# Kernel optimization log

Hardware: AMD Instinct MI355X
Metric: run time of the kernel (lower is better)

The kernel has to match this reference:

```python
import jax, jax.numpy as jnp
import numpy as np

NUM_SPLITS = 4
SPLIT_CH = 4          # 16 channels / 4 splits
N_BRANCH = NUM_SPLITS * 2   # 2 pyramid branches per group
K = 2                 # multi_frequency_compression k
MAX_U, MAX_V = 5, 5
N_CLASSES = 60
LN_EPS = 1e-5


def _conv(x, w):
    # x: [B, Cin, H, W], w: [Cout, Cin, kh, kw], SAME padding, stride 1
    return jax.lax.conv_general_dilated(
        x, w, window_strides=(1, 1), padding='SAME',
        dimension_numbers=('NCHW', 'OIHW', 'NCHW'))


def _branch(x, w3, b3, w5, b5, w7, b7):
    # one PyramidMultiScaleCNN branch: dense 3x3 -> 5x5 -> 7x7 with input re-concat
    a = jax.nn.relu(_conv(x, w3) + b3[None, :, None, None])            # [B,64,H,W]
    b = jax.nn.relu(_conv(jnp.concatenate([a, x], 1), w5) + b5[None, :, None, None])  # [B,128,H,W]
    c = jax.nn.relu(_conv(jnp.concatenate([b, x], 1), w7) + b7[None, :, None, None])  # [B,256,H,W]
    return jnp.concatenate([a, b, c], axis=1)                          # [B,448,H,W]


def _dct_basis(H, W, dtype):
    # first K frequency pairs (u,v) in row-major order of a MAX_U x MAX_V grid
    uv = [(i // MAX_V, i % MAX_V) for i in range(K)]
    u = jnp.array([p[0] for p in uv], dtype=dtype)   # [K]
    v = jnp.array([p[1] for p in uv], dtype=dtype)   # [K]
    h = jnp.arange(H, dtype=dtype) + 0.5
    w = jnp.arange(W, dtype=dtype) + 0.5
    cos_u = jnp.cos(jnp.pi * u[:, None] * h[None, :] / H)  # [K,H]
    cos_v = jnp.cos(jnp.pi * v[:, None] * w[None, :] / W)  # [K,W]
    return cos_u, cos_v


def setup_inputs() -> dict:
    key = jax.random.key(0)
    ks = jax.random.split(key, 16)
    B, C, H, W = 16, 16, 32, 32
    s = 0.02
    x = jax.random.normal(ks[0], (B, C, H, W), jnp.float32)
    # stacked params for the 8 identical-shaped pyramid branches (index = 2*group + branch)
    w3 = jax.random.normal(ks[1], (N_BRANCH, 64, SPLIT_CH, 3, 3), jnp.float32) * s
    b3 = jnp.zeros((N_BRANCH, 64), jnp.float32)
    w5 = jax.random.normal(ks[2], (N_BRANCH, 128, 64 + SPLIT_CH, 5, 5), jnp.float32) * s
    b5 = jnp.zeros((N_BRANCH, 128), jnp.float32)
    w7 = jax.random.normal(ks[3], (N_BRANCH, 256, 128 + SPLIT_CH, 7, 7), jnp.float32) * s
    b7 = jnp.zeros((N_BRANCH, 256), jnp.float32)
    fused_c = N_BRANCH * 448  # 3584
    Wg = jax.random.normal(ks[4], (N_CLASSES, fused_c), jnp.float32) * s
    bg = jnp.zeros((N_CLASSES,), jnp.float32)
    f_dct = fused_c * K       # 7168
    gamma = jnp.ones((f_dct,), jnp.float32)
    beta = jnp.zeros((f_dct,), jnp.float32)
    Wd = jax.random.normal(ks[5], (N_CLASSES, f_dct), jnp.float32) * s
    bd = jnp.zeros((N_CLASSES,), jnp.float32)
    return {"x": x, "w3": w3, "b3": b3, "w5": w5, "b5": b5, "w7": w7, "b7": b7,
            "Wg": Wg, "bg": bg, "gamma": gamma, "beta": beta, "Wd": Wd, "bd": bd}


def reference(x, w3, b3, w5, b5, w7, b7, Wg, bg, gamma, beta, Wd, bd):
    B, C, H, W = x.shape
    # split channels into groups: [NUM_SPLITS, B, SPLIT_CH, H, W]
    parts = x.reshape(B, NUM_SPLITS, SPLIT_CH, H, W).transpose(1, 0, 2, 3, 4)
    # each group feeds 2 branches; branch index i = 2*group + branch matches fused cat order
    xg = jnp.repeat(parts, 2, axis=0)                               # [8,B,SPLIT_CH,H,W]
    outs = jax.vmap(_branch)(xg, w3, b3, w5, b5, w7, b7)            # [8,B,448,H,W]
    fused = outs.transpose(1, 0, 2, 3, 4).reshape(B, N_BRANCH * 448, H, W)  # [B,3584,H,W]

    # GAP head
    gap_feat = fused.mean(axis=(2, 3))                              # [B,3584]
    gap_pred = gap_feat @ Wg.T + bg                                 # [B,60]

    # batched multi-frequency DCT compression (replaces per-sample Python loop)
    cos_u, cos_v = _dct_basis(H, W, fused.dtype)                    # [K,H],[K,W]
    dct = jnp.einsum('bchw,kh,kw->bck', fused, cos_u, cos_v)        # [B,3584,K]
    dct = dct.reshape(B, -1)                                        # [B,7168]

    mu = dct.mean(axis=-1, keepdims=True)
    var = jnp.var(dct, axis=-1, keepdims=True)
    normed = (dct - mu) * jax.lax.rsqrt(var + LN_EPS) * gamma + beta
    # dropout omitted (eval mode)
    dct_pred = normed @ Wd.T + bd                                   # [B,60]
    return (gap_pred, dct_pred)
```

## Files before the change

kernel.cpp:

```cpp
#include <hip/hip_runtime.h>
#include <math.h>

#define PI_F 3.14159265358979323846f

typedef short bf16x8 __attribute__((ext_vector_type(8)));
typedef float f32x4  __attribute__((ext_vector_type(4)));
typedef float f32x16 __attribute__((ext_vector_type(16)));

__device__ __forceinline__ short f2bf(float f) {
    union { float f; unsigned u; } v; v.f = f;
    unsigned r = v.u + 0x7fffu + ((v.u >> 16) & 1u);
    return (short)(r >> 16);
}


__global__ __launch_bounds__(256) void prep_s1in(const float* __restrict__ x, short* __restrict__ dst) {
    int idx = blockIdx.x * 256 + threadIdx.x;
    if (idx >= 64 * 1024) return;
    int px = idx & 1023;
    int g  = (idx >> 10) & 3;
    int b  = idx >> 12;
    short v8[8];
    #pragma unroll
    for (int j = 0; j < 8; ++j) {
        float f = (j < 4) ? x[((b * 16 + g * 4 + j) << 10) + px] : 0.f;
        v8[j] = f2bf(f);
    }
    *(int4*)(dst + (size_t)idx * 8) = *(const int4*)v8;
}

__global__ __launch_bounds__(256) void prep_sx(const float* __restrict__ x, short* __restrict__ dst,
                                               int CHS, int CH0) {
    int idx = blockIdx.x * 256 + threadIdx.x;
    if (idx >= 128 * 1024) return;
    int px = idx & 1023, pair = idx >> 10;
    int i = pair >> 4, b = pair & 15, g = i >> 1;
    short v8[8];
    #pragma unroll
    for (int j = 0; j < 8; ++j) {
        float f = (j < 4) ? x[((b * 16 + g * 4 + j) << 10) + px] : 0.f;
        v8[j] = f2bf(f);
    }
    *(int4*)(dst + (size_t)idx * CHS + CH0) = *(const int4*)v8;
}

template<int KS, int CHS, int CINR, int COUT, int NCH>
__global__ __launch_bounds__(256) void wprep_d(const float* __restrict__ w, short* __restrict__ Bw) {
    constexpr int TOTAL = 8 * KS * NCH * COUT * 4;
    int idx = blockIdx.x * 256 + threadIdx.x;
    if (idx >= TOTAL) return;
    int kb = idx & 3;
    int r  = idx >> 2;
    int n  = r % COUT;  r /= COUT;
    int c  = r % NCH;   r /= NCH;
    int kh = r % KS;
    int br = r / KS;
    short v8[8];
    #pragma unroll
    for (int j = 0; j < 8; ++j) {
        int k   = c * 32 + kb * 8 + j;
        int kwc = k / CHS;
        int ch  = k - kwc * CHS;
        float f = (kwc < KS && ch < CINR)
                ? w[(((size_t)br * COUT + n) * CINR + ch) * (KS * KS) + kh * KS + kwc] : 0.f;
        v8[j] = f2bf(f);
    }
    *(int4*)(Bw + (size_t)idx * 8) = *(const int4*)v8;
}

template<int KS, int CHS, int COUT, int CHS_OUT, int FOFF, bool S1SRC>
__global__ __launch_bounds__(512, 2) void conv_hk(
    const short* __restrict__ sIn,
    short* __restrict__ sOut,
    const short* __restrict__ Bw,
    const float* __restrict__ bias,
    float* __restrict__ sums)
{
    constexpr int PAD    = KS / 2;
    constexpr int NCH    = (KS * CHS + 31) / 32;
    constexpr int TCX    = 32 + (NCH * 32 - 1) / CHS;
    constexpr int NSLOT  = 9;
    constexpr int NFN    = COUT / 64;
    constexpr int CPP    = CHS / 8;
    constexpr int RCHK   = TCX * CPP;
    constexpr int CHUNKB = COUT * 32;
    static_assert(NCH == 1 || (NCH % 2) == 0, "NCH must be 1 or even");

    __shared__ int4 AtileV[(NSLOT * TCX * CHS) / 8];
    short* Atile = (short*)AtileV;

    const int t    = threadIdx.x;
    const int lane = t & 63, w = t >> 6;
    const int wm = w >> 2, wn = w & 3;
    const int lm = lane & 15, kb = lane >> 4;

    const int bid = blockIdx.x;
    const int i  = bid & 7;
    const int b  = (bid >> 3) & 15;
    const int mt = bid >> 7;
    const int r0 = mt * 8;

    const int pairPx = (i * 16 + b) << 10;
    const int srcPx  = S1SRC ? ((b * 4 + (i >> 1)) << 10) : pairPx;

    int nIdx[NFN], nOff[NFN];
    #pragma unroll
    for (int fn = 0; fn < NFN; ++fn) {
        nIdx[fn] = wn * (COUT / 4) + fn * 16 + lm;
        nOff[fn] = nIdx[fn] * 32 + kb * 8;
    }

    f32x4 acc[8][NFN];
    #pragma unroll
    for (int fm = 0; fm < 8; ++fm)
        #pragma unroll
        for (int fn = 0; fn < NFN; ++fn)
            acc[fm][fn] = (f32x4){0.f, 0.f, 0.f, 0.f};

    const short* Bp = Bw + (size_t)i * KS * NCH * CHUNKB;
    bf16x8 b0[NFN], b1[NFN];
    #pragma unroll
    for (int fn = 0; fn < NFN; ++fn)
        b0[fn] = *(const bf16x8*)(Bp + nOff[fn]);

    for (int e = t; e < 9 * RCHK; e += 512) {
        int j  = e / RCHK, e2 = e - j * RCHK;
        int tc = e2 / CPP, kc = e2 - tc * CPP;
        int rin = r0 - PAD + j, cin = tc - PAD;
        int4 v = {0, 0, 0, 0};
        if (rin >= 0 && rin < 32 && cin >= 0 && cin < 32)
            v = *(const int4*)(sIn + (size_t)(srcPx + rin * 32 + cin) * CHS + kc * 8);
        *(int4*)(Atile + (j * TCX + tc) * CHS + kc * 8) = v;
    }
    __syncthreads();

    for (int kh = 0; kh < KS; ++kh) {
        int aB[8];
        #pragma unroll
        for (int fm = 0; fm < 8; ++fm) {
            int slot = kh + wm * 4 + (fm >> 1);
            if (slot >= NSLOT) slot -= NSLOT;
            aB[fm] = (slot * TCX + (fm & 1) * 16 + lm) * CHS + kb * 8;
        }

        const bool doStage = (kh <= KS - 3);
        const int stRin = r0 - PAD + kh + 9;
        int4 stg0 = {0, 0, 0, 0};
        if (doStage) {
            if (t < RCHK) {
                int tc = t / CPP, kc = t - tc * CPP;
                int cin = tc - PAD;
                if (stRin >= 0 && stRin < 32 && cin >= 0 && cin < 32)
                    stg0 = *(const int4*)(sIn + (size_t)(srcPx + stRin * 32 + cin) * CHS + kc * 8);
            }
        }

        if constexpr (NCH == 1) {
            __builtin_amdgcn_s_setprio(1);
            #pragma unroll
            for (int fm = 0; fm < 8; ++fm) {
                bf16x8 af = *(const bf16x8*)(Atile + aB[fm]);
                #pragma unroll
                for (int fn = 0; fn < NFN; ++fn)
                    acc[fm][fn] = __builtin_amdgcn_mfma_f32_16x16x32_bf16(af, b0[fn], acc[fm][fn], 0, 0, 0);
            }
            __builtin_amdgcn_s_setprio(0);
            if (kh < KS - 1) {
                #pragma unroll
                for (int fn = 0; fn < NFN; ++fn)
                    b0[fn] = *(const bf16x8*)(Bp + CHUNKB + nOff[fn]);
            }
            Bp += CHUNKB;
        } else {
            #pragma unroll 1
            for (int c = 0; c < NCH; c += 2) {
                #pragma unroll
                for (int fn = 0; fn < NFN; ++fn)
                    b1[fn] = *(const bf16x8*)(Bp + (size_t)(c + 1) * CHUNKB + nOff[fn]);
                __builtin_amdgcn_s_setprio(1);
                #pragma unroll
                for (int fm = 0; fm < 8; ++fm) {
                    bf16x8 af = *(const bf16x8*)(Atile + aB[fm] + c * 32);
                    #pragma unroll
                    for (int fn = 0; fn < NFN; ++fn)
                        acc[fm][fn] = __builtin_amdgcn_mfma_f32_16x16x32_bf16(af, b0[fn], acc[fm][fn], 0, 0, 0);
                }
                __builtin_amdgcn_s_setprio(0);
                if (!(kh == KS - 1 && c + 2 >= NCH)) {
                    #pragma unroll
                    for (int fn = 0; fn < NFN; ++fn)
                        b0[fn] = *(const bf16x8*)(Bp + (size_t)(c + 2) * CHUNKB + nOff[fn]);
                }
                __builtin_amdgcn_s_setprio(1);
                #pragma unroll
                for (int fm = 0; fm < 8; ++fm) {
                    bf16x8 af = *(const bf16x8*)(Atile + aB[fm] + (c + 1) * 32);
                    #pragma unroll
                    for (int fn = 0; fn < NFN; ++fn)
                        acc[fm][fn] = __builtin_amdgcn_mfma_f32_16x16x32_bf16(af, b1[fn], acc[fm][fn], 0, 0, 0);
                }
                __builtin_amdgcn_s_setprio(0);
            }
            Bp += (size_t)NCH * CHUNKB;
        }

        __syncthreads();
        if (doStage) {
            if (t < RCHK) {
                int tc = t / CPP, kc = t - tc * CPP;
                *(int4*)(Atile + (kh * TCX + tc) * CHS + kc * 8) = stg0;
            }
        }
    }

    float cwv[2][4];
    #pragma unroll
    for (int half = 0; half < 2; ++half)
        #pragma unroll
        for (int r = 0; r < 4; ++r)
            cwv[half][r] = cosf(PI_F * (half * 16 + kb * 4 + r + 0.5f) / 32.f);

    #pragma unroll
    for (int fn = 0; fn < NFN; ++fn) {
        int n = nIdx[fn];
        float bv = bias[i * COUT + n];
        float s0 = 0.f, s1 = 0.f;
        #pragma unroll
        for (int fm = 0; fm < 8; ++fm) {
            int imgrow = wm * 4 + (fm >> 1);
            int half = fm & 1;
            #pragma unroll
            for (int r = 0; r < 4; ++r) {
                float v = fmaxf(acc[fm][fn][r] + bv, 0.f);
                if constexpr (CHS_OUT > 0) {
                    int col = half * 16 + kb * 4 + r;
                    int R = r0 + imgrow;
                    sOut[(size_t)(pairPx + R * 32 + col) * CHS_OUT + n] = f2bf(v);
                }
                s0 += v;
                s1 += v * cwv[half][r];
            }
        }
        s0 += __shfl_xor(s0, 16); s1 += __shfl_xor(s1, 16);
        s0 += __shfl_xor(s0, 32); s1 += __shfl_xor(s1, 32);
        if (kb == 0) {
            int ch = i * 448 + FOFF + n;
            atomicAdd(&sums[((size_t)b * 3584 + ch) * 2 + 0], s0);
            atomicAdd(&sums[((size_t)b * 3584 + ch) * 2 + 1], s1);
        }
    }
}

template<int KS, int CHS, int COUT, int CHS_OUT, int FOFF>
__global__ __launch_bounds__(512, 2) void conv_hk32(
    const short* __restrict__ sIn,
    short* __restrict__ sOut,
    const short* __restrict__ Bw,
    const float* __restrict__ bias,
    float* __restrict__ sums)
{
    constexpr int PAD    = KS / 2;
    constexpr int NCH    = (KS * CHS + 31) / 32;
    constexpr int TCX    = 32 + (NCH * 32 - 1) / CHS;
    constexpr int NSLOT  = 9;
    constexpr int NFN    = COUT / 128;
    constexpr int CPP    = CHS / 8;
    constexpr int RCHK   = TCX * CPP;
    constexpr int CHUNKB = COUT * 32;
    static_assert((NCH % 2) == 0, "NCH must be even");

    __shared__ int4 AtileV[(NSLOT * TCX * CHS) / 8];
    char* Alds = (char*)AtileV;

    const int t    = threadIdx.x;
    const int lane = t & 63, w = t >> 6;
    const int wm = w >> 2, wn = w & 3;
    const int ln = lane & 31, hi = lane >> 5;

    const int bid = blockIdx.x;
    const int i  = bid & 7;
    const int b  = (bid >> 3) & 15;
    const int mt = bid >> 7;
    const int r0 = mt * 8;
    const int pairPx = (i * 16 + b) << 10;

    int nIdx[NFN], nOff[NFN];
    #pragma unroll
    for (int fn = 0; fn < NFN; ++fn) {
        nIdx[fn] = wn * (COUT / 4) + fn * 32 + ln;
        nOff[fn] = nIdx[fn] * 32 + hi * 8;
    }

    f32x16 acc[4][NFN];
    #pragma unroll
    for (int mf = 0; mf < 4; ++mf)
        #pragma unroll
        for (int fn = 0; fn < NFN; ++fn)
            acc[mf][fn] = (f32x16)(0.f);

    const short* Bp = Bw + (size_t)i * KS * NCH * CHUNKB;
    bf16x8 b0[NFN][2], b1[NFN][2];
    #pragma unroll
    for (int fn = 0; fn < NFN; ++fn) {
        b0[fn][0] = *(const bf16x8*)(Bp + nOff[fn]);
        b0[fn][1] = *(const bf16x8*)(Bp + nOff[fn] + 16);
    }

    for (int e = t; e < 9 * RCHK; e += 512) {
        int j  = e / RCHK, e2 = e - j * RCHK;
        int tc = e2 / CPP, kc = e2 - tc * CPP;
        int rin = r0 - PAD + j, cin = tc - PAD;
        int4 v = {0, 0, 0, 0};
        if (rin >= 0 && rin < 32 && cin >= 0 && cin < 32)
            v = *(const int4*)(sIn + (size_t)(pairPx + rin * 32 + cin) * CHS + kc * 8);
        int off = ((j * TCX + tc) * CHS + kc * 8) * 2;
        off ^= ((off >> 7) & 1) << 4;
        *(int4*)(Alds + off) = v;
    }
    __syncthreads();

    for (int kh = 0; kh < KS; ++kh) {
        int aB[4];
        #pragma unroll
        for (int mf = 0; mf < 4; ++mf) {
            int slot = kh + wm * 4 + mf;
            if (slot >= NSLOT) slot -= NSLOT;
            aB[mf] = (slot * TCX + ln) * CHS * 2 + hi * 16;
        }

        const bool doStage = (kh <= KS - 3);
        const int stRin = r0 - PAD + kh + 9;
        int4 stg0 = {0, 0, 0, 0}, stg1 = {0, 0, 0, 0};
        if (doStage) {
            if (t < RCHK) {
                int tc = t / CPP, kc = t - tc * CPP;
                int cin = tc - PAD;
                if (stRin >= 0 && stRin < 32 && cin >= 0 && cin < 32)
                    stg0 = *(const int4*)(sIn + (size_t)(pairPx + stRin * 32 + cin) * CHS + kc * 8);
            }
            if constexpr (RCHK > 512) {
                int e2 = t + 512;
                if (e2 < RCHK) {
                    int tc = e2 / CPP, kc = e2 - tc * CPP;
                    int cin = tc - PAD;
                    if (stRin >= 0 && stRin < 32 && cin >= 0 && cin < 32)
                        stg1 = *(const int4*)(sIn + (size_t)(pairPx + stRin * 32 + cin) * CHS + kc * 8);
                }
            }
        }

        #pragma unroll 1
        for (int c = 0; c < NCH; c += 2) {
            #pragma unroll
            for (int fn = 0; fn < NFN; ++fn) {
                b1[fn][0] = *(const bf16x8*)(Bp + (size_t)(c + 1) * CHUNKB + nOff[fn]);
                b1[fn][1] = *(const bf16x8*)(Bp + (size_t)(c + 1) * CHUNKB + nOff[fn] + 16);
            }
            __builtin_amdgcn_s_setprio(1);
            #pragma unroll
            for (int kk = 0; kk < 2; ++kk) {
                #pragma unroll
                for (int mf = 0; mf < 4; ++mf) {
                    int off = aB[mf] + c * 64 + kk * 32;
                    off ^= ((off >> 7) & 1) << 4;
                    bf16x8 af = *(const bf16x8*)(Alds + off);
                    #pragma unroll
                    for (int fn = 0; fn < NFN; ++fn)
                        acc[mf][fn] = __builtin_amdgcn_mfma_f32_32x32x16_bf16(af, b0[fn][kk], acc[mf][fn], 0, 0, 0);
                }
            }
            __builtin_amdgcn_s_setprio(0);
            if (!(kh == KS - 1 && c + 2 >= NCH)) {
                #pragma unroll
                for (int fn = 0; fn < NFN; ++fn) {
                    b0[fn][0] = *(const bf16x8*)(Bp + (size_t)(c + 2) * CHUNKB + nOff[fn]);
                    b0[fn][1] = *(const bf16x8*)(Bp + (size_t)(c + 2) * CHUNKB + nOff[fn] + 16);
                }
            }
            __builtin_amdgcn_s_setprio(1);
            #pragma unroll
            for (int kk = 0; kk < 2; ++kk) {
                #pragma unroll
                for (int mf = 0; mf < 4; ++mf) {
                    int off = aB[mf] + (c + 1) * 64 + kk * 32;
                    off ^= ((off >> 7) & 1) << 4;
                    bf16x8 af = *(const bf16x8*)(Alds + off);
                    #pragma unroll
                    for (int fn = 0; fn < NFN; ++fn)
                        acc[mf][fn] = __builtin_amdgcn_mfma_f32_32x32x16_bf16(af, b1[fn][kk], acc[mf][fn], 0, 0, 0);
                }
            }
            __builtin_amdgcn_s_setprio(0);
        }
        Bp += (size_t)NCH * CHUNKB;

        __syncthreads();
        if (doStage) {
            if (t < RCHK) {
                int tc = t / CPP, kc = t - tc * CPP;
                int off = ((kh * TCX + tc) * CHS + kc * 8) * 2;
                off ^= ((off >> 7) & 1) << 4;
                *(int4*)(Alds + off) = stg0;
            }
            if constexpr (RCHK > 512) {
                int e2 = t + 512;
                if (e2 < RCHK) {
                    int tc = e2 / CPP, kc = e2 - tc * CPP;
                    int off = ((kh * TCX + tc) * CHS + kc * 8) * 2;
                    off ^= ((off >> 7) & 1) << 4;
                    *(int4*)(Alds + off) = stg1;
                }
            }
        }
    }

    float cw[16];
    #pragma unroll
    for (int r = 0; r < 16; ++r) {
        int px = (r & 3) + 8 * (r >> 2) + 4 * hi;
        cw[r] = cosf(PI_F * (px + 0.5f) / 32.f);
    }

    #pragma unroll
    for (int fn = 0; fn < NFN; ++fn) {
        int n = nIdx[fn];
        float bv = bias[i * COUT + n];
        float s0 = 0.f, s1 = 0.f;
        #pragma unroll
        for (int mf = 0; mf < 4; ++mf) {
            int R = r0 + wm * 4 + mf;
            #pragma unroll
            for (int r = 0; r < 16; ++r) {
                float v = fmaxf(acc[mf][fn][r] + bv, 0.f);
                if constexpr (CHS_OUT > 0) {
                    int px = (r & 3) + 8 * (r >> 2) + 4 * hi;
                    sOut[(size_t)(pairPx + R * 32 + px) * CHS_OUT + n] = f2bf(v);
                }
                s0 += v;
                s1 += v * cw[r];
            }
        }
        s0 += __shfl_xor(s0, 32);
        s1 += __shfl_xor(s1, 32);
        if (hi == 0) {
            int ch = i * 448 + FOFF + n;
            atomicAdd(&sums[((size_t)b * 3584 + ch) * 2 + 0], s0);
            atomicAdd(&sums[((size_t)b * 3584 + ch) * 2 + 1], s1);
        }
    }
}

__global__ __launch_bounds__(256) void ln_stats(const float* __restrict__ sums,
                                                float* __restrict__ stats) {
    __shared__ float red[8];
    const int b = blockIdx.x;
    const int t = threadIdx.x, lane = t & 63, wv = t >> 6;
    const float* S = sums + (size_t)b * 7168;
    float ls = 0.f, lq = 0.f;
    for (int f = t; f < 7168; f += 256) { float v = S[f]; ls += v; lq += v * v; }
    for (int m = 1; m < 64; m <<= 1) { ls += __shfl_xor(ls, m); lq += __shfl_xor(lq, m); }
    if (lane == 0) { red[wv] = ls; red[4 + wv] = lq; }
    __syncthreads();
    if (t == 0) {
        float ts = red[0] + red[1] + red[2] + red[3];
        float tq = red[4] + red[5] + red[6] + red[7];
        float mu  = ts * (1.f / 7168.f);
        float var = tq * (1.f / 7168.f) - mu * mu;
        stats[b * 2 + 0] = mu;
        stats[b * 2 + 1] = rsqrtf(var + 1e-5f);
    }
}

__global__ __launch_bounds__(256) void head_gemv(
    const float* __restrict__ sums,
    const float* __restrict__ stats,
    const float* __restrict__ Wg, const float* __restrict__ bg,
    const float* __restrict__ gamma, const float* __restrict__ beta,
    const float* __restrict__ Wd, const float* __restrict__ bd,
    float* __restrict__ out)
{
    __shared__ float red[8];
    const int n = blockIdx.x % 60;
    const int b = blockIdx.x / 60;
    const int t = threadIdx.x, lane = t & 63, wv = t >> 6;
    const float* S  = sums + (size_t)b * 7168;
    const float mu  = stats[b * 2 + 0];
    const float inv = stats[b * 2 + 1];

    const float* wd = Wd + (size_t)n * 7168;
    float accd = 0.f;
    for (int f = t; f < 7168; f += 256) {
        float v = (S[f] - mu) * inv * gamma[f] + beta[f];
        accd = fmaf(v, wd[f], accd);
    }
    const float* wg = Wg + (size_t)n * 3584;
    float accg = 0.f;
    for (int ch = t; ch < 3584; ch += 256)
        accg = fmaf(S[2 * ch], wg[ch], accg);

    for (int m = 1; m < 64; m <<= 1) { accg += __shfl_xor(accg, m); accd += __shfl_xor(accd, m); }
    if (lane == 0) { red[wv] = accg; red[4 + wv] = accd; }
    __syncthreads();
    if (t == 0) {
        float g = red[0] + red[1] + red[2] + red[3];
        float d = red[4] + red[5] + red[6] + red[7];
        out[b * 60 + n]       = g * (1.f / 1024.f) + bg[n];
        out[960 + b * 60 + n] = d + bd[n];
    }
}

extern "C" void kernel_launch(void* const* d_in, const int* in_sizes, int n_in,
                              void* d_out, int out_size, void* d_ws, size_t ws_size,
                              hipStream_t stream)
{
    const float* x     = (const float*)d_in[0];
    const float* w3    = (const float*)d_in[1];
    const float* b3    = (const float*)d_in[2];
    const float* w5    = (const float*)d_in[3];
    const float* b5    = (const float*)d_in[4];
    const float* w7    = (const float*)d_in[5];
    const float* b7    = (const float*)d_in[6];
    const float* Wg    = (const float*)d_in[7];
    const float* bg    = (const float*)d_in[8];
    const float* gamma = (const float*)d_in[9];
    const float* beta  = (const float*)d_in[10];
    const float* Wd    = (const float*)d_in[11];
    const float* bd    = (const float*)d_in[12];
    float* out = (float*)d_out;

    char* p = (char*)d_ws;
    float* sums  = (float*)p;             p += 458752;
    float* stats = (float*)p;             p += 128;
    short* s1in = (short*)p;              p += 1048576;
    short* s2in = (short*)p;              p += 18874368;
    short* s3in = (short*)p;              p += 35651584;
    short* Bw3  = (short*)p;              p += 98304;
    short* Bw5  = (short*)p;              p += 3932160;
    short* Bw7  = (short*)p;              p += 27525120;

    hipMemsetAsync(sums, 0, 458752, stream);
    prep_s1in<<<dim3(256), dim3(256), 0, stream>>>(x, s1in);
    prep_sx<<<dim3(512), dim3(256), 0, stream>>>(x, s2in, 72, 64);
    prep_sx<<<dim3(512), dim3(256), 0, stream>>>(x, s3in, 136, 128);
    wprep_d<3, 8, 4, 64, 1><<<dim3(24), dim3(256), 0, stream>>>(w3, Bw3);
    wprep_d<5, 72, 68, 128, 12><<<dim3(960), dim3(256), 0, stream>>>(w5, Bw5);
    wprep_d<7, 136, 132, 256, 30><<<dim3(6720), dim3(256), 0, stream>>>(w7, Bw7);

    conv_hk<3, 8, 64, 72, 0, true><<<dim3(512), dim3(512), 0, stream>>>(s1in, s2in, Bw3, b3, sums);
    conv_hk32<5, 72, 128, 136, 64><<<dim3(512), dim3(512), 0, stream>>>(s2in, s3in, Bw5, b5, sums);
    conv_hk32<7, 136, 256, 0, 192><<<dim3(512), dim3(512), 0, stream>>>(s3in, nullptr, Bw7, b7, sums);

    ln_stats<<<dim3(16), dim3(256), 0, stream>>>(sums, stats);
    head_gemv<<<dim3(960), dim3(256), 0, stream>>>(sums, stats, Wg, bg, gamma, beta, Wd, bd, out);
}
```

Before: 516.5 us.

## Pre-pad and pre-swizzle conv7 input in global memory, load via global_load_lds

The 5x5 conv now writes its output into a zero-padded, LDS-swizzled global layout (38 rows of 11264 bytes per image pair), so the 7x7 conv can copy whole rows straight into LDS with global_load_lds and skip bounds checks and register staging. The 5x5 layer moves from the 32x32 MFMA kernel to the 16x16 conv_hk variant, and both conv kernels double-buffer A fragments from LDS so reads overlap with MFMAs. The cost is a 55MB memset of the padded buffer and scattered 2-byte writes in the conv5 epilogue.

```diff
diff --git a/kernel.cpp b/kernel.cpp
--- a/kernel.cpp
+++ b/kernel.cpp
@@ -11,6 +11,12 @@
     union { float f; unsigned u; } v; v.f = f;
     unsigned r = v.u + 0x7fffu + ((v.u >> 16) & 1u);
     return (short)(r >> 16);
+}
+
+__device__ __forceinline__ void gld16(const short* g, short* l) {
+    __builtin_amdgcn_global_load_lds(
+        (const __attribute__((address_space(1))) unsigned int*)g,
+        (__attribute__((address_space(3))) unsigned int*)l, 16, 0, 0);
 }
 
 
@@ -42,6 +48,23 @@
         v8[j] = f2bf(f);
     }
     *(int4*)(dst + (size_t)idx * CHS + CH0) = *(const int4*)v8;
+}
+
+__global__ __launch_bounds__(256) void prep_s3x(const float* __restrict__ x, short* __restrict__ dst) {
+    int idx = blockIdx.x * 256 + threadIdx.x;
+    if (idx >= 128 * 1024) return;
+    int px = idx & 1023, pair = idx >> 10;
+    int i = pair >> 4, b = pair & 15, g = i >> 1;
+    int R = px >> 5, C = px & 31;
+    short v8[8];
+    #pragma unroll
+    for (int j = 0; j < 8; ++j) {
+        float f = (j < 4) ? x[((b * 16 + g * 4 + j) << 10) + px] : 0.f;
+        v8[j] = f2bf(f);
+    }
+    int p = ((C + 3) * 136 + 128) * 2;
+    p ^= ((p >> 7) & 1) << 4;
+    *(int4*)((char*)dst + ((size_t)pair * 38 + R + 3) * 11264 + p) = *(const int4*)v8;
 }
 
 template<int KS, int CHS, int CINR, int COUT, int NCH>
@@ -68,7 +91,7 @@
     *(int4*)(Bw + (size_t)idx * 8) = *(const int4*)v8;
 }
 
-template<int KS, int CHS, int COUT, int CHS_OUT, int FOFF, bool S1SRC>
+template<int KS, int CHS, int COUT, int CHS_OUT, int FOFF, bool S1SRC, bool POUT>
 __global__ __launch_bounds__(512, 2) void conv_hk(
     const short* __restrict__ sIn,
     short* __restrict__ sOut,
@@ -85,6 +108,7 @@
     constexpr int RCHK   = TCX * CPP;
     constexpr int CHUNKB = COUT * 32;
     static_assert(NCH == 1 || (NCH % 2) == 0, "NCH must be 1 or even");
+    static_assert(RCHK <= 512, "single stg reg");
 
     __shared__ int4 AtileV[(NSLOT * TCX * CHS) / 8];
     short* Atile = (short*)AtileV;
@@ -100,7 +124,8 @@
     const int mt = bid >> 7;
     const int r0 = mt * 8;
 
-    const int pairPx = (i * 16 + b) << 10;
+    const int pairIdx = i * 16 + b;
+    const int pairPx = pairIdx << 10;
     const int srcPx  = S1SRC ? ((b * 4 + (i >> 1)) << 10) : pairPx;
 
     int nIdx[NFN], nOff[NFN];
@@ -134,8 +159,10 @@
     }
     __syncthreads();
 
+    bf16x8 aP[4], aQ[4];
+    int aB[8];
+
     for (int kh = 0; kh < KS; ++kh) {
-        int aB[8];
         #pragma unroll
         for (int fm = 0; fm < 8; ++fm) {
             int slot = kh + wm * 4 + (fm >> 1);
@@ -172,44 +199,57 @@
             }
             Bp += CHUNKB;
         } else {
+            auto LD4 = [&](bf16x8 (&dst)[4], int c, int mb) {
+                #pragma unroll
+                for (int j = 0; j < 4; ++j)
+                    dst[j] = *(const bf16x8*)(Atile + aB[mb + j] + c * 32);
+            };
+            auto MM4L = [&](bf16x8 (&a)[4], bf16x8 (&bb)[NFN]) {
+                __builtin_amdgcn_s_setprio(1);
+                #pragma unroll
+                for (int j = 0; j < 4; ++j)
+                    #pragma unroll
+                    for (int fn = 0; fn < NFN; ++fn)
+                        acc[j][fn] = __builtin_amdgcn_mfma_f32_16x16x32_bf16(a[j], bb[fn], acc[j][fn], 0, 0, 0);
+                __builtin_amdgcn_s_setprio(0);
+            };
+            auto MM4H = [&](bf16x8 (&a)[4], bf16x8 (&bb)[NFN]) {
+                __builtin_amdgcn_s_setprio(1);
+                #pragma unroll
+                for (int j = 0; j < 4; ++j)
+                    #pragma unroll
+                    for (int fn = 0; fn < NFN; ++fn)
+                        acc[4 + j][fn] = __builtin_amdgcn_mfma_f32_16x16x32_bf16(a[j], bb[fn], acc[4 + j][fn], 0, 0, 0);
+                __builtin_amdgcn_s_setprio(0);
+            };
+
+            LD4(aP, 0, 0);
             #pragma unroll 1
             for (int c = 0; c < NCH; c += 2) {
                 #pragma unroll
                 for (int fn = 0; fn < NFN; ++fn)
                     b1[fn] = *(const bf16x8*)(Bp + (size_t)(c + 1) * CHUNKB + nOff[fn]);
-                __builtin_amdgcn_s_setprio(1);
-                #pragma unroll
-                for (int fm = 0; fm < 8; ++fm) {
-                    bf16x8 af = *(const bf16x8*)(Atile + aB[fm] + c * 32);
-                    #pragma unroll
-                    for (int fn = 0; fn < NFN; ++fn)
-                        acc[fm][fn] = __builtin_amdgcn_mfma_f32_16x16x32_bf16(af, b0[fn], acc[fm][fn], 0, 0, 0);
-                }
-                __builtin_amdgcn_s_setprio(0);
+                LD4(aQ, c, 4);
+                MM4L(aP, b0);
+                LD4(aP, c + 1, 0);
+                MM4H(aQ, b0);
                 if (!(kh == KS - 1 && c + 2 >= NCH)) {
                     #pragma unroll
                     for (int fn = 0; fn < NFN; ++fn)
                         b0[fn] = *(const bf16x8*)(Bp + (size_t)(c + 2) * CHUNKB + nOff[fn]);
                 }
-                __builtin_amdgcn_s_setprio(1);
-                #pragma unroll
-                for (int fm = 0; fm < 8; ++fm) {
-                    bf16x8 af = *(const bf16x8*)(Atile + aB[fm] + (c + 1) * 32);
-                    #pragma unroll
-                    for (int fn = 0; fn < NFN; ++fn)
-                        acc[fm][fn] = __builtin_amdgcn_mfma_f32_16x16x32_bf16(af, b1[fn], acc[fm][fn], 0, 0, 0);
-                }
-                __builtin_amdgcn_s_setprio(0);
+                LD4(aQ, c + 1, 4);
+                MM4L(aP, b1);
+                if (c + 2 < NCH) LD4(aP, c + 2, 0);
+                MM4H(aQ, b1);
             }
             Bp += (size_t)NCH * CHUNKB;
         }
 
         __syncthreads();
-        if (doStage) {
-            if (t < RCHK) {
-                int tc = t / CPP, kc = t - tc * CPP;
-                *(int4*)(Atile + (kh * TCX + tc) * CHS + kc * 8) = stg0;
-            }
+        if (doStage && t < RCHK) {
+            int tc = t / CPP, kc = t - tc * CPP;
+            *(int4*)(Atile + (kh * TCX + tc) * CHS + kc * 8) = stg0;
         }
     }
 
@@ -232,9 +272,13 @@
             #pragma unroll
             for (int r = 0; r < 4; ++r) {
                 float v = fmaxf(acc[fm][fn][r] + bv, 0.f);
-                if constexpr (CHS_OUT > 0) {
-                    int col = half * 16 + kb * 4 + r;
-                    int R = r0 + imgrow;
+                int col = half * 16 + kb * 4 + r;
+                int R = r0 + imgrow;
+                if constexpr (POUT) {
+                    int p = ((col + 3) * CHS_OUT + n) * 2;
+                    p ^= ((p >> 7) & 1) << 4;
+                    *(short*)((char*)sOut + ((size_t)pairIdx * 38 + R + 3) * 11264 + p) = f2bf(v);
+                } else if constexpr (CHS_OUT > 0) {
                     sOut[(size_t)(pairPx + R * 32 + col) * CHS_OUT + n] = f2bf(v);
                 }
                 s0 += v;
@@ -251,26 +295,18 @@
     }
 }
 
-template<int KS, int CHS, int COUT, int CHS_OUT, int FOFF>
-__global__ __launch_bounds__(512, 2) void conv_hk32(
-    const short* __restrict__ sIn,
-    short* __restrict__ sOut,
+__global__ __launch_bounds__(512, 2) void conv7_mfma(
+    const short* __restrict__ sPad,
     const short* __restrict__ Bw,
     const float* __restrict__ bias,
     float* __restrict__ sums)
 {
-    constexpr int PAD    = KS / 2;
-    constexpr int NCH    = (KS * CHS + 31) / 32;
-    constexpr int TCX    = 32 + (NCH * 32 - 1) / CHS;
-    constexpr int NSLOT  = 9;
-    constexpr int NFN    = COUT / 128;
-    constexpr int CPP    = CHS / 8;
-    constexpr int RCHK   = TCX * CPP;
+    constexpr int NCH = 30, NFN = 2, COUT = 256;
+    constexpr int RSTR = 5632;
     constexpr int CHUNKB = COUT * 32;
-    static_assert((NCH % 2) == 0, "NCH must be even");
-
-    __shared__ int4 AtileV[(NSLOT * TCX * CHS) / 8];
-    char* Alds = (char*)AtileV;
+
+    __shared__ int4 AldsV[(9 * RSTR) / 8];
+    short* Alds = (short*)AldsV;
 
     const int t    = threadIdx.x;
     const int lane = t & 63, w = t >> 6;
@@ -282,12 +318,12 @@
     const int b  = (bid >> 3) & 15;
     const int mt = bid >> 7;
     const int r0 = mt * 8;
-    const int pairPx = (i * 16 + b) << 10;
+    const size_t sBase = (size_t)(i * 16 + b) * 38 * RSTR;
 
     int nIdx[NFN], nOff[NFN];
     #pragma unroll
     for (int fn = 0; fn < NFN; ++fn) {
-        nIdx[fn] = wn * (COUT / 4) + fn * 32 + ln;
+        nIdx[fn] = wn * 64 + fn * 32 + ln;
         nOff[fn] = nIdx[fn] * 32 + hi * 8;
     }
 
@@ -298,7 +334,7 @@
         for (int fn = 0; fn < NFN; ++fn)
             acc[mf][fn] = (f32x16)(0.f);
 
-    const short* Bp = Bw + (size_t)i * KS * NCH * CHUNKB;
+    const short* Bp = Bw + (size_t)i * 7 * NCH * CHUNKB;
     bf16x8 b0[NFN][2], b1[NFN][2];
     #pragma unroll
     for (int fn = 0; fn < NFN; ++fn) {
@@ -306,49 +342,43 @@
         b0[fn][1] = *(const bf16x8*)(Bp + nOff[fn] + 16);
     }
 
-    for (int e = t; e < 9 * RCHK; e += 512) {
-        int j  = e / RCHK, e2 = e - j * RCHK;
-        int tc = e2 / CPP, kc = e2 - tc * CPP;
-        int rin = r0 - PAD + j, cin = tc - PAD;
-        int4 v = {0, 0, 0, 0};
-        if (rin >= 0 && rin < 32 && cin >= 0 && cin < 32)
-            v = *(const int4*)(sIn + (size_t)(pairPx + rin * 32 + cin) * CHS + kc * 8);
-        int off = ((j * TCX + tc) * CHS + kc * 8) * 2;
-        off ^= ((off >> 7) & 1) << 4;
-        *(int4*)(Alds + off) = v;
+    for (int s = w; s < 99; s += 8) {
+        int j = s / 11, sg = s - j * 11;
+        gld16(sPad + sBase + (size_t)(r0 + j) * RSTR + sg * 512 + lane * 8,
+              Alds + j * RSTR + sg * 512 + lane * 8);
     }
     __syncthreads();
 
-    for (int kh = 0; kh < KS; ++kh) {
-        int aB[4];
+    bf16x8 aP[4], aQ[4];
+    int aB[4];
+
+    for (int kh = 0; kh < 7; ++kh) {
         #pragma unroll
         for (int mf = 0; mf < 4; ++mf) {
             int slot = kh + wm * 4 + mf;
-            if (slot >= NSLOT) slot -= NSLOT;
-            aB[mf] = (slot * TCX + ln) * CHS * 2 + hi * 16;
-        }
-
-        const bool doStage = (kh <= KS - 3);
-        const int stRin = r0 - PAD + kh + 9;
-        int4 stg0 = {0, 0, 0, 0}, stg1 = {0, 0, 0, 0};
-        if (doStage) {
-            if (t < RCHK) {
-                int tc = t / CPP, kc = t - tc * CPP;
-                int cin = tc - PAD;
-                if (stRin >= 0 && stRin < 32 && cin >= 0 && cin < 32)
-                    stg0 = *(const int4*)(sIn + (size_t)(pairPx + stRin * 32 + cin) * CHS + kc * 8);
-            }
-            if constexpr (RCHK > 512) {
-                int e2 = t + 512;
-                if (e2 < RCHK) {
-                    int tc = e2 / CPP, kc = e2 - tc * CPP;
-                    int cin = tc - PAD;
-                    if (stRin >= 0 && stRin < 32 && cin >= 0 && cin < 32)
-                        stg1 = *(const int4*)(sIn + (size_t)(pairPx + stRin * 32 + cin) * CHS + kc * 8);
-                }
-            }
-        }
-
+            if (slot >= 9) slot -= 9;
+            aB[mf] = slot * (RSTR * 2) + ln * 272 + hi * 16;
+        }
+
+        auto LDA = [&](bf16x8 (&dst)[4], int c, int kk) {
+            #pragma unroll
+            for (int mf = 0; mf < 4; ++mf) {
+                int off = aB[mf] + c * 64 + kk * 32;
+                off ^= ((off >> 7) & 1) << 4;
+                dst[mf] = *(const bf16x8*)((const char*)Alds + off);
+            }
+        };
+        auto MM = [&](bf16x8 (&a)[4], bf16x8 &q0, bf16x8 &q1) {
+            __builtin_amdgcn_s_setprio(1);
+            #pragma unroll
+            for (int mf = 0; mf < 4; ++mf) {
+                acc[mf][0] = __builtin_amdgcn_mfma_f32_32x32x16_bf16(a[mf], q0, acc[mf][0], 0, 0, 0);
+                acc[mf][1] = __builtin_amdgcn_mfma_f32_32x32x16_bf16(a[mf], q1, acc[mf][1], 0, 0, 0);
+            }
+            __builtin_amdgcn_s_setprio(0);
+        };
+
+        LDA(aP, 0, 0);
         #pragma unroll 1
         for (int c = 0; c < NCH; c += 2) {
             #pragma unroll
@@ -356,61 +386,30 @@
                 b1[fn][0] = *(const bf16x8*)(Bp + (size_t)(c + 1) * CHUNKB + nOff[fn]);
                 b1[fn][1] = *(const bf16x8*)(Bp + (size_t)(c + 1) * CHUNKB + nOff[fn] + 16);
             }
-            __builtin_amdgcn_s_setprio(1);
-            #pragma unroll
-            for (int kk = 0; kk < 2; ++kk) {
-                #pragma unroll
-                for (int mf = 0; mf < 4; ++mf) {
-                    int off = aB[mf] + c * 64 + kk * 32;
-                    off ^= ((off >> 7) & 1) << 4;
-                    bf16x8 af = *(const bf16x8*)(Alds + off);
-                    #pragma unroll
-                    for (int fn = 0; fn < NFN; ++fn)
-                        acc[mf][fn] = __builtin_amdgcn_mfma_f32_32x32x16_bf16(af, b0[fn][kk], acc[mf][fn], 0, 0, 0);
-                }
-            }
-            __builtin_amdgcn_s_setprio(0);
-            if (!(kh == KS - 1 && c + 2 >= NCH)) {
+            LDA(aQ, c, 1);
+            MM(aP, b0[0][0], b0[1][0]);
+            LDA(aP, c + 1, 0);
+            MM(aQ, b0[0][1], b0[1][1]);
+            if (!(kh == 6 && c + 2 >= NCH)) {
                 #pragma unroll
                 for (int fn = 0; fn < NFN; ++fn) {
                     b0[fn][0] = *(const bf16x8*)(Bp + (size_t)(c + 2) * CHUNKB + nOff[fn]);
                     b0[fn][1] = *(const bf16x8*)(Bp + (size_t)(c + 2) * CHUNKB + nOff[fn] + 16);
                 }
             }
-            __builtin_amdgcn_s_setprio(1);
-            #pragma unroll
-            for (int kk = 0; kk < 2; ++kk) {
-                #pragma unroll
-                for (int mf = 0; mf < 4; ++mf) {
-                    int off = aB[mf] + (c + 1) * 64 + kk * 32;
-                    off ^= ((off >> 7) & 1) << 4;
-                    bf16x8 af = *(const bf16x8*)(Alds + off);
-                    #pragma unroll
-                    for (int fn = 0; fn < NFN; ++fn)
-                        acc[mf][fn] = __builtin_amdgcn_mfma_f32_32x32x16_bf16(af, b1[fn][kk], acc[mf][fn], 0, 0, 0);
-                }
-            }
-            __builtin_amdgcn_s_setprio(0);
+            LDA(aQ, c + 1, 1);
+            MM(aP, b1[0][0], b1[1][0]);
+            if (c + 2 < NCH) LDA(aP, c + 2, 0);
+            MM(aQ, b1[0][1], b1[1][1]);
         }
         Bp += (size_t)NCH * CHUNKB;
 
         __syncthreads();
-        if (doStage) {
-            if (t < RCHK) {
-                int tc = t / CPP, kc = t - tc * CPP;
-                int off = ((kh * TCX + tc) * CHS + kc * 8) * 2;
-                off ^= ((off >> 7) & 1) << 4;
-                *(int4*)(Alds + off) = stg0;
-            }
-            if constexpr (RCHK > 512) {
-                int e2 = t + 512;
-                if (e2 < RCHK) {
-                    int tc = e2 / CPP, kc = e2 - tc * CPP;
-                    int off = ((kh * TCX + tc) * CHS + kc * 8) * 2;
-                    off ^= ((off >> 7) & 1) << 4;
-                    *(int4*)(Alds + off) = stg1;
-                }
-            }
+        if (kh <= 4) {
+            size_t rb = sBase + (size_t)(r0 + kh + 9) * RSTR;
+            for (int s = w; s < 11; s += 8)
+                gld16(sPad + rb + s * 512 + lane * 8,
+                      Alds + kh * RSTR + s * 512 + lane * 8);
         }
     }
 
@@ -428,14 +427,9 @@
         float s0 = 0.f, s1 = 0.f;
         #pragma unroll
         for (int mf = 0; mf < 4; ++mf) {
-            int R = r0 + wm * 4 + mf;
             #pragma unroll
             for (int r = 0; r < 16; ++r) {
                 float v = fmaxf(acc[mf][fn][r] + bv, 0.f);
-                if constexpr (CHS_OUT > 0) {
-                    int px = (r & 3) + 8 * (r >> 2) + 4 * hi;
-                    sOut[(size_t)(pairPx + R * 32 + px) * CHS_OUT + n] = f2bf(v);
-                }
                 s0 += v;
                 s1 += v * cw[r];
             }
@@ -443,7 +437,7 @@
         s0 += __shfl_xor(s0, 32);
         s1 += __shfl_xor(s1, 32);
         if (hi == 0) {
-            int ch = i * 448 + FOFF + n;
+            int ch = i * 448 + 192 + n;
             atomicAdd(&sums[((size_t)b * 3584 + ch) * 2 + 0], s0);
             atomicAdd(&sums[((size_t)b * 3584 + ch) * 2 + 1], s1);
         }
@@ -531,24 +525,25 @@
     char* p = (char*)d_ws;
     float* sums  = (float*)p;             p += 458752;
     float* stats = (float*)p;             p += 128;
-    short* s1in = (short*)p;              p += 1048576;
-    short* s2in = (short*)p;              p += 18874368;
-    short* s3in = (short*)p;              p += 35651584;
-    short* Bw3  = (short*)p;              p += 98304;
-    short* Bw5  = (short*)p;              p += 3932160;
-    short* Bw7  = (short*)p;              p += 27525120;
+    short* s1in  = (short*)p;             p += 1048576;
+    short* s2in  = (short*)p;             p += 18874368;
+    short* s3pad = (short*)p;             p += 54788096;
+    short* Bw3   = (short*)p;             p += 98304;
+    short* Bw5   = (short*)p;             p += 3932160;
+    short* Bw7   = (short*)p;             p += 27525120;
 
     hipMemsetAsync(sums, 0, 458752, stream);
+    hipMemsetAsync(s3pad, 0, 54788096, stream);
     prep_s1in<<<dim3(256), dim3(256), 0, stream>>>(x, s1in);
     prep_sx<<<dim3(512), dim3(256), 0, stream>>>(x, s2in, 72, 64);
-    prep_sx<<<dim3(512), dim3(256), 0, stream>>>(x, s3in, 136, 128);
+    prep_s3x<<<dim3(512), dim3(256), 0, stream>>>(x, s3pad);
     wprep_d<3, 8, 4, 64, 1><<<dim3(24), dim3(256), 0, stream>>>(w3, Bw3);
     wprep_d<5, 72, 68, 128, 12><<<dim3(960), dim3(256), 0, stream>>>(w5, Bw5);
     wprep_d<7, 136, 132, 256, 30><<<dim3(6720), dim3(256), 0, stream>>>(w7, Bw7);
 
-    conv_hk<3, 8, 64, 72, 0, true><<<dim3(512), dim3(512), 0, stream>>>(s1in, s2in, Bw3, b3, sums);
-    conv_hk32<5, 72, 128, 136, 64><<<dim3(512), dim3(512), 0, stream>>>(s2in, s3in, Bw5, b5, sums);
-    conv_hk32<7, 136, 256, 0, 192><<<dim3(512), dim3(512), 0, stream>>>(s3in, nullptr, Bw7, b7, sums);
+    conv_hk<3, 8, 64, 72, 0, true, false><<<dim3(512), dim3(512), 0, stream>>>(s1in, s2in, Bw3, b3, sums);
+    conv_hk<5, 72, 128, 136, 64, false, true><<<dim3(512), dim3(512), 0, stream>>>(s2in, s3pad, Bw5, b5, sums);
+    conv7_mfma<<<dim3(512), dim3(512), 0, stream>>>(s3pad, Bw7, b7, sums);
 
     ln_stats<<<dim3(16), dim3(256), 0, stream>>>(sums, stats);
     head_gemv<<<dim3(960), dim3(256), 0, stream>>>(sums, stats, Wg, bg, gamma, beta, Wd, bd, out);
```

Result: slower. 552.0 us (+6.9%).
